# Kernel optimization log

Hardware: AMD Instinct MI355X
Metric: run time of the kernel (lower is better)

The kernel has to match this reference:

```python
import jax, jax.numpy as jnp
import numpy as np

B, P = 4, 2048
N = B * P
QD = 512            # query_dim == inner_dim (pos_emb is added to raw features)
CD = 512            # context_dim
HEADS, DH = 8, 64
INNER = HEADS * DH
SCALE = DH ** -0.5
HC, WC = 32, 32     # context spatial grid
L = HC * WC         # context_len
SELF_HW = 512       # spatial_dim[:2]
STRIDE = 8          # resolution_level == sparse tensor stride
PE_H = SELF_HW // STRIDE  # 64 BEV pos-emb grid


def setup_inputs() -> dict:
    key = jax.random.key(0)
    k = jax.random.split(key, 9)
    return {
        "feats": jax.random.normal(k[0], (N, QD), jnp.float32),
        "coords_xy": jax.random.randint(k[1], (N, 2), 0, SELF_HW),
        "context_emb": jax.random.normal(k[2], (B, HC, WC, CD), jnp.float32),
        "Wq": jax.random.normal(k[3], (QD, INNER), jnp.float32) * 0.02,
        "Wk": jax.random.normal(k[4], (CD, INNER), jnp.float32) * 0.02,
        "Wv": jax.random.normal(k[5], (CD, INNER), jnp.float32) * 0.02,
        "Wo": jax.random.normal(k[6], (INNER, QD), jnp.float32) * 0.02,
        "bo": jnp.zeros((QD,), jnp.float32),
        "pos_embedding": jax.random.normal(k[7], (PE_H, PE_H, INNER), jnp.float32) / INNER ** 0.5,
        "context_pos_embedding": jax.random.normal(k[8], (L, CD), jnp.float32) / INNER ** 0.5,
    }


def _neighbor_mask(coords_xy):
    # get_context_mask: scatter a (2*STRIDE+1)^2 neighborhood around each point's
    # projected context cell into a [N, L] boolean mask
    ratio = jnp.float32(HC) / jnp.float32(SELF_HW)
    center = jnp.round(coords_xy.astype(jnp.float32) * ratio).astype(jnp.int32)  # [N,2]
    off = jnp.stack(
        jnp.meshgrid(jnp.arange(-STRIDE, STRIDE + 1), jnp.arange(-STRIDE, STRIDE + 1), indexing="ij"),
        axis=-1,
    ).reshape(-1, 2)  # [K,2], K = 289
    pos = center[:, None, :] + off[None, :, :]        # [N,K,2]
    r = jnp.clip(pos[..., 0], 0, HC - 1)
    c = jnp.clip(pos[..., 1], 0, WC - 1)
    flat = r * WC + c                                  # [N,K]
    return jnp.zeros((N, L), jnp.bool_).at[jnp.arange(N)[:, None], flat].set(True)


def reference(feats, coords_xy, context_emb, Wq, Wk, Wv, Wo, bo, pos_embedding, context_pos_embedding):
    # get_context: add learned context positional embedding, flatten spatial -> [B, L, CD]
    ctx = (context_emb + context_pos_embedding.reshape(HC, WC, CD)).reshape(B, L, CD)
    # get_pos_emb: gather BEV positional embedding per point via floor(coord/stride)
    rc = coords_xy // STRIDE                           # [N,2] in [0, 64)
    pe = pos_embedding[rc[:, 0], rc[:, 1]]             # [N, INNER]
    f = (feats + pe).reshape(B, P, QD)                 # points grouped per batch (equal counts)
    mask = _neighbor_mask(coords_xy).reshape(B, P, L)
    q = (f @ Wq).reshape(B, P, HEADS, DH).transpose(0, 2, 1, 3)    # [B,h,P,d]
    k = (ctx @ Wk).reshape(B, L, HEADS, DH).transpose(0, 2, 1, 3)  # [B,h,L,d]
    v = (ctx @ Wv).reshape(B, L, HEADS, DH).transpose(0, 2, 1, 3)
    sim = jnp.einsum("bhid,bhjd->bhij", q, k) * SCALE              # [B,h,P,L]
    neg = -jnp.finfo(sim.dtype).max
    sim = jnp.where(mask[:, None, :, :], sim, neg)
    attn = jax.nn.softmax(sim, axis=-1)
    out = jnp.einsum("bhij,bhjd->bhid", attn, v)
    out = out.transpose(0, 2, 1, 3).reshape(B, P, INNER)
    out = out @ Wo + bo                                # to_out (dropout=0, eval)
    return out.reshape(N, QD)                          # scatter back to point features
```

## Files before the change

kernel.cpp:

```cpp
#include <hip/hip_runtime.h>


typedef __attribute__((ext_vector_type(8))) short bf16x8;
typedef __attribute__((ext_vector_type(4))) float f32x4;

#define SCL 0.18033688f

__device__ __forceinline__ unsigned short f2bf(float x) {
  union { float f; unsigned int u; } v; v.f = x;
  unsigned int r = v.u + 0x7FFFu + ((v.u >> 16) & 1u);
  return (unsigned short)(r >> 16);
}

__device__ __forceinline__ unsigned int pk2bf(float a, float b) {
  return (unsigned)f2bf(a) | ((unsigned)f2bf(b) << 16);
}

__device__ __forceinline__ unsigned int cvtpk(float a, float b) {
  unsigned int r;
  asm("v_cvt_pk_bf16_f32 %0, %1, %2" : "=v"(r) : "v"(a), "v"(b));
  return r;
}

__device__ __forceinline__ float fexp2(float x) {
#if __has_builtin(__builtin_amdgcn_exp2f)
  return __builtin_amdgcn_exp2f(x);
#else
  return exp2f(x);
#endif
}

__device__ __forceinline__ void gload16(const unsigned short* g, char* l) {
  __builtin_amdgcn_global_load_lds(
      (const __attribute__((address_space(1))) unsigned int*)g,
      (__attribute__((address_space(3))) unsigned int*)l, 16, 0, 0);
}

__device__ __forceinline__ int swzb(int row, int chk) {
  return row * 128 + ((chk * 16) ^ ((row & 7) << 4));
}

__global__ __launch_bounds__(256) void prep_w(const float* __restrict__ Wq, const float* __restrict__ Wk,
                                              const float* __restrict__ Wv, const float* __restrict__ Wo,
                                              unsigned short* __restrict__ Wqt, unsigned short* __restrict__ Wkt,
                                              unsigned short* __restrict__ Wvt, unsigned short* __restrict__ Wot) {
  __shared__ float tile[64][65];
  const int bid = blockIdx.x;
  const int wsel = bid >> 6, tt = bid & 63;
  const int kt = (tt >> 3) << 6, ntb = (tt & 7) << 6;
  const float* W = (wsel == 0) ? Wq : (wsel == 1) ? Wk : (wsel == 2) ? Wv : Wo;
  unsigned short* Wt = (wsel == 0) ? Wqt : (wsel == 1) ? Wkt : (wsel == 2) ? Wvt : Wot;
  const int t = threadIdx.x;
#pragma unroll
  for (int p = 0; p < 16; ++p) {
    int e = p * 256 + t;
    int row = e >> 6, col = e & 63;
    tile[row][col] = W[(long)(kt + row) * 512 + ntb + col];
  }
  __syncthreads();
#pragma unroll
  for (int p = 0; p < 16; ++p) {
    int e = p * 256 + t;
    int n = e >> 6, k = e & 63;
    Wt[(long)(ntb + n) * 512 + kt + k] = f2bf(tile[k][n]);
  }
}

__global__ __launch_bounds__(256) void prep_in(const float* __restrict__ feats,
                                               const int* __restrict__ coords,
                                               const float* __restrict__ pos_emb,
                                               const float* __restrict__ ctx,
                                               const float* __restrict__ ctx_pos,
                                               unsigned short* __restrict__ Aq,
                                               unsigned short* __restrict__ Ac,
                                               int* __restrict__ perm) {
  if (blockIdx.x >= 6144) {
    __shared__ int hist[64];
    __shared__ int base[64];
    const int bb = blockIdx.x - 6144;
    const int t = threadIdx.x;
    if (t < 64) hist[t] = 0;
    __syncthreads();
    int keys[8];
#pragma unroll
    for (int i = 0; i < 8; ++i) {
      int q = bb * 2048 + t * 8 + i;
      int cr = (int)rintf((float)coords[2 * q] * 0.0625f);
      keys[i] = cr;
      atomicAdd(&hist[cr], 1);
    }
    __syncthreads();
    if (t == 0) {
      int s = 0;
      for (int k2 = 0; k2 < 64; ++k2) { base[k2] = s; s += hist[k2]; }
    }
    __syncthreads();
#pragma unroll
    for (int i = 0; i < 8; ++i) {
      int pos = atomicAdd(&base[keys[i]], 1);
      perm[bb * 2048 + pos] = t * 8 + i;
    }
    return;
  }
  int i = blockIdx.x * 256 + threadIdx.x;
  if (i < 1048576) {
    int e = i << 2;
    int q = e >> 9, k = e & 511;
    int pi = ((coords[2 * q] >> 3) << 6) + (coords[2 * q + 1] >> 3);
    float4 a = *(const float4*)(feats + e);
    float4 p = *(const float4*)(pos_emb + ((size_t)pi << 9) + k);
    uint2 o;
    o.x = pk2bf(a.x + p.x, a.y + p.y);
    o.y = pk2bf(a.z + p.z, a.w + p.w);
    *(uint2*)(Aq + e) = o;
  } else {
    int e = (i - 1048576) << 2;
    int r = e >> 9, k = e & 511;
    float4 a = *(const float4*)(ctx + e);
    float4 p = *(const float4*)(ctx_pos + ((size_t)(r & 1023) << 9) + k);
    uint2 o;
    o.x = pk2bf(a.x + p.x, a.y + p.y);
    o.y = pk2bf(a.z + p.z, a.w + p.w);
    *(uint2*)(Ac + e) = o;
  }
}

__global__ __launch_bounds__(256) void gemm_qkv(const unsigned short* __restrict__ Aq,
                                                const unsigned short* __restrict__ Ac,
                                                const unsigned short* __restrict__ Wqt,
                                                const unsigned short* __restrict__ Wkt,
                                                const unsigned short* __restrict__ Wvt,
                                                unsigned short* __restrict__ Qb,
                                                unsigned short* __restrict__ Kb,
                                                unsigned short* __restrict__ Vt) {
  __shared__ char Asf[2][16384];
  __shared__ char Bsf[2][16384];
  const int t = threadIdx.x, l = t & 63, wv = t >> 6;
  const int wr = (wv >> 1) << 6, wc = (wv & 1) << 6;
  const int orig = blockIdx.x;
  const int bx = (orig & 7) * 64 + (orig >> 3);
  const bool isQ = bx < 256;
  long tm; const unsigned short* Bt; const unsigned short* Ab; bool isV = false; int nt;
  if (isQ) {
    tm = (long)(bx >> 2) * 128;
    nt = bx & 3;
    Bt = Wqt + (long)nt * 65536;
    Ab = Aq;
  } else {
    const int kvx = bx - 256;
    tm = (long)(kvx >> 3) * 128;
    const int y = kvx & 7;
    isV = y >= 4; nt = y & 3;
    Bt = (isV ? Wvt : Wkt) + (long)nt * 65536;
    Ab = Ac;
  }

  const int rr = l >> 3, chs = (l & 7) ^ rr;
  auto STAGE = [&](int buf, int k0) {
#pragma unroll
    for (int i = 0; i < 4; ++i) {
      int c = (wv << 2) + i;
      int row = (c << 3) + rr;
      gload16(Ab + (tm + row) * 512 + k0 + chs * 8, Asf[buf] + (c << 10));
      gload16(Bt + (long)row * 512 + k0 + chs * 8, Bsf[buf] + (c << 10));
    }
  };

  STAGE(0, 0);
  __syncthreads();

  f32x4 acc[4][4] = {};
  const int lr = l & 15, g = l >> 4;

  for (int s = 0; s < 8; ++s) {
    const int cur = s & 1;
    if (s < 7) STAGE(cur ^ 1, (s + 1) << 6);
#pragma unroll
    for (int kk = 0; kk < 2; ++kk) {
      const int chd = (kk << 2) + g;
      bf16x8 af[4], bfr[4];
#pragma unroll
      for (int i = 0; i < 4; ++i) {
        int ra = wr + i * 16 + lr;
        int rb = wc + i * 16 + lr;
        af[i]  = *(const bf16x8*)(Asf[cur] + swzb(ra, chd));
        bfr[i] = *(const bf16x8*)(Bsf[cur] + swzb(rb, chd));
      }
#pragma unroll
      for (int mi = 0; mi < 4; ++mi)
#pragma unroll
        for (int ni = 0; ni < 4; ++ni)
          acc[mi][ni] = __builtin_amdgcn_mfma_f32_16x16x32_bf16(af[mi], bfr[ni], acc[mi][ni], 0, 0, 0);
    }
    __syncthreads();
  }

  const int lq = g << 2;
#pragma unroll
  for (int mi = 0; mi < 4; ++mi)
#pragma unroll
    for (int ni = 0; ni < 4; ++ni) {
      int cn = nt * 128 + wc + ni * 16 + lr;
      long r0 = tm + wr + mi * 16 + lq;
      if (isQ) {
#pragma unroll
        for (int r = 0; r < 4; ++r)
          Qb[(r0 + r) * 512 + cn] = f2bf(acc[mi][ni][r] * SCL);
      } else if (!isV) {
#pragma unroll
        for (int r = 0; r < 4; ++r)
          Kb[(r0 + r) * 512 + cn] = f2bf(acc[mi][ni][r]);
      } else {
        int h = cn >> 6, d = cn & 63;
#pragma unroll
        for (int r = 0; r < 4; ++r) {
          long row = r0 + r;
          int b = (int)(row >> 10), j = (int)(row & 1023);
          int jp = (j & ~63) | ((j & 15) << 2) | ((j >> 4) & 3);
          Vt[((long)(b * 8 + h) * 64 + d) * 1024 + jp] = f2bf(acc[mi][ni][r]);
        }
      }
    }
}

__global__ __launch_bounds__(512, 4) void attn_mfma(const unsigned short* __restrict__ Qb,
                                                    const unsigned short* __restrict__ Kb,
                                                    const unsigned short* __restrict__ Vt,
                                                    const int* __restrict__ coords,
                                                    const int* __restrict__ perm,
                                                    unsigned short* __restrict__ Abf) {
  __shared__ char Kl[2][8192];
  __shared__ char Vl[2][8192];
  __shared__ char Ol[2048];
  __shared__ unsigned short Plds[8][16][72];
  __shared__ int permL[128];
  __shared__ int rng[2];
  const int t = threadIdx.x, w = t >> 6, l = t & 63;
  const int g = l >> 4, lc = l & 15;
  const int orig = blockIdx.x;
  const int sw = (orig & 7) * 64 + (orig >> 3);
  const int qx = sw & 15, bh = sw >> 4;
  const int b = bh >> 3, h = bh & 7;

  if (t < 128) permL[t] = perm[b * 2048 + qx * 128 + t];
  if (t == 0) { rng[0] = 63; rng[1] = 0; }
  __syncthreads();

  int rm[4], cm[4];
  int lrmin = 63, lrmax = 0;
#pragma unroll
  for (int r = 0; r < 4; ++r) {
    long qq = (long)b * 2048 + permL[w * 16 + g * 4 + r];
    int cr = (int)rintf((float)coords[2 * qq] * 0.0625f);
    int cc = (int)rintf((float)coords[2 * qq + 1] * 0.0625f);
    int rlo = max(0, cr - 8), rhi = min(31, cr + 8);
    int clo = max(0, cc - 8), chi = min(31, cc + 8);
    rm[r] = (int)((((unsigned)1 << (rhi - rlo + 1)) - 1) << rlo);
    cm[r] = (int)((((unsigned)1 << (chi - clo + 1)) - 1) << clo);
    lrmin = min(lrmin, rlo); lrmax = max(lrmax, rhi);
  }
#pragma unroll
  for (int off = 32; off > 0; off >>= 1) {
    lrmin = min(lrmin, __shfl_xor(lrmin, off));
    lrmax = max(lrmax, __shfl_xor(lrmax, off));
  }
  const int wt0 = lrmin >> 1, wt1 = lrmax >> 1;
  if (l == 0) { atomicMin(&rng[0], lrmin); atomicMax(&rng[1], lrmax); }

  bf16x8 qfr[2];
  {
    long qrow = (long)b * 2048 + permL[w * 16 + lc];
#pragma unroll
    for (int dc = 0; dc < 2; ++dc)
      qfr[dc] = *(const bf16x8*)(Qb + qrow * 512 + h * 64 + dc * 32 + g * 8);
  }

  const int srow = t >> 3, schk = t & 7;
  const unsigned short* Kg = Kb + ((long)b * 1024) * 512 + h * 64;
  const unsigned short* Vg = Vt + ((long)bh * 64) * 1024;

  if (t < 128) {
    int r = t >> 3, c = t & 7;
    unsigned short vv = (r == 0) ? (unsigned short)0x3F80 : (unsigned short)0;
    unsigned short tmp[8] = {vv, vv, vv, vv, vv, vv, vv, vv};
    *(int4*)(Ol + swzb(r, c)) = *(int4*)tmp;
  }
  __syncthreads();
  const int t0 = rng[0] >> 1, t1 = rng[1] >> 1;
  {
    const int kb0 = t0 * 64;
    int4 sk = *(const int4*)(Kg + (long)(kb0 + srow) * 512 + schk * 8);
    int4 sv_ = *(const int4*)(Vg + (long)srow * 1024 + kb0 + schk * 8);
    *(int4*)(Kl[0] + swzb(srow, schk)) = sk;
    *(int4*)(Vl[0] + swzb(srow, schk)) = sv_;
  }
  __syncthreads();

  f32x4 po[5] = {};

  for (int kt = t0; kt <= t1; ++kt) {
    const int cur = (kt - t0) & 1;
    const int kb = kt * 64;
    int4 nk = {}, nv = {};
    if (kt < t1) {
      const int kbn = kb + 64;
      nk = *(const int4*)(Kg + (long)(kbn + srow) * 512 + schk * 8);
      nv = *(const int4*)(Vg + (long)srow * 1024 + kbn + schk * 8);
    }

    if (kt >= wt0 && kt <= wt1) {
      bf16x8 kfr[4][2];
#pragma unroll
      for (int kf = 0; kf < 4; ++kf)
#pragma unroll
        for (int dc = 0; dc < 2; ++dc)
          kfr[kf][dc] = *(const bf16x8*)(Kl[cur] + swzb(kf * 16 + lc, dc * 4 + g));

      f32x4 sv[4];
#pragma unroll
      for (int kf = 0; kf < 4; ++kf) {
        f32x4 a = {};
        a = __builtin_amdgcn_mfma_f32_16x16x32_bf16(qfr[0], kfr[kf][0], a, 0, 0, 0);
        a = __builtin_amdgcn_mfma_f32_16x16x32_bf16(qfr[1], kfr[kf][1], a, 0, 0, 0);
        sv[kf] = a;
      }

      const int jrb = kb >> 5;
      int cmk[4][4];
#pragma unroll
      for (int kf = 0; kf < 4; ++kf) {
        int jr = jrb + (kf >> 1);
#pragma unroll
        for (int r = 0; r < 4; ++r)
          cmk[kf][r] = ((rm[r] >> jr) & 1) ? cm[r] : 0;
      }
#pragma unroll
      for (int kf = 0; kf < 4; ++kf) {
        int jc = ((kf & 1) << 4) + lc;
#pragma unroll
        for (int r = 0; r < 4; ++r) {
          float p = fexp2(sv[kf][r]);
          sv[kf][r] = ((cmk[kf][r] >> jc) & 1) ? p : 0.0f;
        }
      }

      bf16x8 vfr[5][2];
#pragma unroll
      for (int df = 0; df < 4; ++df)
#pragma unroll
        for (int kc = 0; kc < 2; ++kc)
          vfr[df][kc] = *(const bf16x8*)(Vl[cur] + swzb(df * 16 + lc, kc * 4 + g));
#pragma unroll
      for (int kc = 0; kc < 2; ++kc)
        vfr[4][kc] = *(const bf16x8*)(Ol + swzb(lc, kc * 4 + g));

#pragma unroll
      for (int r = 0; r < 4; ++r) {
        uint2 pk;
        pk.x = cvtpk(sv[0][r], sv[1][r]);
        pk.y = cvtpk(sv[2][r], sv[3][r]);
        *(uint2*)(&Plds[w][g * 4 + r][4 * lc]) = pk;
      }

      bf16x8 pa0 = *(const bf16x8*)(&Plds[w][lc][g * 8]);
      bf16x8 pa1 = *(const bf16x8*)(&Plds[w][lc][32 + g * 8]);
      __builtin_amdgcn_s_setprio(1);
#pragma unroll
      for (int df = 0; df < 5; ++df) {
        po[df] = __builtin_amdgcn_mfma_f32_16x16x32_bf16(pa0, vfr[df][0], po[df], 0, 0, 0);
        po[df] = __builtin_amdgcn_mfma_f32_16x16x32_bf16(pa1, vfr[df][1], po[df], 0, 0, 0);
      }
      __builtin_amdgcn_s_setprio(0);
    }

    if (kt < t1) {
      const int nxt = cur ^ 1;
      *(int4*)(Kl[nxt] + swzb(srow, schk)) = nk;
      *(int4*)(Vl[nxt] + swzb(srow, schk)) = nv;
    }
    __syncthreads();
  }

#pragma unroll
  for (int r = 0; r < 4; ++r) {
    float lsum = __shfl(po[4][r], l & 48);
    float inv = 1.0f / lsum;
    long qr = (long)b * 2048 + permL[w * 16 + g * 4 + r];
#pragma unroll
    for (int df = 0; df < 4; ++df)
      Abf[qr * 512 + h * 64 + df * 16 + lc] = f2bf(po[df][r] * inv);
  }
}

__global__ __launch_bounds__(256) void gemm_o(const unsigned short* __restrict__ A,
                                              const unsigned short* __restrict__ Bt,
                                              float* __restrict__ C,
                                              const float* __restrict__ bias) {
  __shared__ char Asf[2][8192];
  __shared__ char Bsf[2][16384];
  const int t = threadIdx.x, l = t & 63, wv = t >> 6;
  const int wr = (wv >> 1) << 5;
  const int wc = (wv & 1) << 6;
  const int orig = blockIdx.x;
  const int bx = (orig & 7) * 64 + (orig >> 3);
  const long tm = (long)(bx >> 2) * 64;
  const long tn = (long)(bx & 3) * 128;

  const int rr = l >> 3, chs = (l & 7) ^ rr;
  auto STAGE = [&](int buf, int k0) {
#pragma unroll
    for (int i = 0; i < 2; ++i) {
      int c = (wv << 1) + i;
      int row = (c << 3) + rr;
      gload16(A + (tm + row) * 512 + k0 + chs * 8, Asf[buf] + (c << 10));
    }
#pragma unroll
    for (int i = 0; i < 4; ++i) {
      int c = (wv << 2) + i;
      int row = (c << 3) + rr;
      gload16(Bt + (tn + row) * 512 + k0 + chs * 8, Bsf[buf] + (c << 10));
    }
  };

  STAGE(0, 0);
  __syncthreads();

  f32x4 acc[2][4] = {};
  const int lr = l & 15, g = l >> 4;

  for (int s = 0; s < 8; ++s) {
    const int cur = s & 1;
    if (s < 7) STAGE(cur ^ 1, (s + 1) << 6);
#pragma unroll
    for (int kk = 0; kk < 2; ++kk) {
      const int chd = (kk << 2) + g;
      bf16x8 af[2], bfr[4];
#pragma unroll
      for (int i = 0; i < 2; ++i)
        af[i] = *(const bf16x8*)(Asf[cur] + swzb(wr + i * 16 + lr, chd));
#pragma unroll
      for (int i = 0; i < 4; ++i)
        bfr[i] = *(const bf16x8*)(Bsf[cur] + swzb(wc + i * 16 + lr, chd));
#pragma unroll
      for (int mi = 0; mi < 2; ++mi)
#pragma unroll
        for (int ni = 0; ni < 4; ++ni)
          acc[mi][ni] = __builtin_amdgcn_mfma_f32_16x16x32_bf16(af[mi], bfr[ni], acc[mi][ni], 0, 0, 0);
    }
    __syncthreads();
  }

  const int lq = g << 2;
#pragma unroll
  for (int mi = 0; mi < 2; ++mi)
#pragma unroll
    for (int ni = 0; ni < 4; ++ni) {
      long col = tn + wc + ni * 16 + lr;
      float bv = bias[col];
      long r0 = tm + wr + mi * 16 + lq;
#pragma unroll
      for (int r = 0; r < 4; ++r)
        C[(r0 + r) * 512 + col] = acc[mi][ni][r] + bv;
    }
}

extern "C" void kernel_launch(void* const* d_in, const int* in_sizes, int n_in,
                              void* d_out, int out_size, void* d_ws, size_t ws_size,
                              hipStream_t stream) {
  (void)in_sizes; (void)n_in; (void)out_size; (void)ws_size;
  const float* feats   = (const float*)d_in[0];
  const int*   coords  = (const int*)d_in[1];
  const float* ctx     = (const float*)d_in[2];
  const float* Wq      = (const float*)d_in[3];
  const float* Wk      = (const float*)d_in[4];
  const float* Wv      = (const float*)d_in[5];
  const float* Wo      = (const float*)d_in[6];
  const float* bo      = (const float*)d_in[7];
  const float* pos_emb = (const float*)d_in[8];
  const float* ctx_pos = (const float*)d_in[9];
  float* out = (float*)d_out;
  char* ws = (char*)d_ws;

  unsigned short* Wqt = (unsigned short*)(ws);
  unsigned short* Wkt = (unsigned short*)(ws + 524288);
  unsigned short* Wvt = (unsigned short*)(ws + 1048576);
  unsigned short* Wot = (unsigned short*)(ws + 1572864);
  unsigned short* Aq  = (unsigned short*)(ws + 2097152);
  unsigned short* Ac  = (unsigned short*)(ws + 10485760);
  unsigned short* Qb  = (unsigned short*)(ws + 14680064);
  unsigned short* Kb  = (unsigned short*)(ws + 23068672);
  unsigned short* Vt  = (unsigned short*)(ws + 27262976);
  unsigned short* Abf = (unsigned short*)(ws + 31457280);
  int*            prm = (int*)(ws + 39845888);

  prep_w  <<<256, 256, 0, stream>>>(Wq, Wk, Wv, Wo, Wqt, Wkt, Wvt, Wot);
  prep_in <<<6148, 256, 0, stream>>>(feats, coords, pos_emb, ctx, ctx_pos, Aq, Ac, prm);
  gemm_qkv<<<512, 256, 0, stream>>>(Aq, Ac, Wqt, Wkt, Wvt, Qb, Kb, Vt);
  attn_mfma<<<512, 512, 0, stream>>>(Qb, Kb, Vt, coords, prm, Abf);
  gemm_o  <<<512, 256, 0, stream>>>(Abf, Wot, out, bo);
}
```

Baseline: 80.69 us.

## Merge prep kernels, halve GEMM K-tile to 32, and raise MFMA priority in attention

Fuses the weight-transpose and input-prep kernels into a single launch to save one kernel launch and its tail. Both GEMMs now stage K tiles of 32 instead of 64 through LDS, with a new 4-row swizzle. This halves shared memory use, which may allow more blocks per CU, but doubles the number of loop iterations and barriers. The attention QK MFMA section is wrapped in s_setprio to favour matrix issue.

```diff
diff --git a/kernel.cpp b/kernel.cpp
--- a/kernel.cpp
+++ b/kernel.cpp
@@ -39,46 +39,49 @@
 __device__ __forceinline__ int swzb(int row, int chk) {
   return row * 128 + ((chk * 16) ^ ((row & 7) << 4));
 }
-
-__global__ __launch_bounds__(256) void prep_w(const float* __restrict__ Wq, const float* __restrict__ Wk,
-                                              const float* __restrict__ Wv, const float* __restrict__ Wo,
-                                              unsigned short* __restrict__ Wqt, unsigned short* __restrict__ Wkt,
-                                              unsigned short* __restrict__ Wvt, unsigned short* __restrict__ Wot) {
-  __shared__ float tile[64][65];
+__device__ __forceinline__ int swz32(int row, int chk) {
+  return row * 64 + ((chk << 4) ^ ((row & 3) << 4));
+}
+
+__global__ __launch_bounds__(256) void prep_all(const float* __restrict__ Wq, const float* __restrict__ Wk,
+                                                const float* __restrict__ Wv, const float* __restrict__ Wo,
+                                                const float* __restrict__ feats,
+                                                const int* __restrict__ coords,
+                                                const float* __restrict__ pos_emb,
+                                                const float* __restrict__ ctx,
+                                                const float* __restrict__ ctx_pos,
+                                                unsigned short* __restrict__ Wqt, unsigned short* __restrict__ Wkt,
+                                                unsigned short* __restrict__ Wvt, unsigned short* __restrict__ Wot,
+                                                unsigned short* __restrict__ Aq,
+                                                unsigned short* __restrict__ Ac,
+                                                int* __restrict__ perm) {
   const int bid = blockIdx.x;
-  const int wsel = bid >> 6, tt = bid & 63;
-  const int kt = (tt >> 3) << 6, ntb = (tt & 7) << 6;
-  const float* W = (wsel == 0) ? Wq : (wsel == 1) ? Wk : (wsel == 2) ? Wv : Wo;
-  unsigned short* Wt = (wsel == 0) ? Wqt : (wsel == 1) ? Wkt : (wsel == 2) ? Wvt : Wot;
   const int t = threadIdx.x;
-#pragma unroll
-  for (int p = 0; p < 16; ++p) {
-    int e = p * 256 + t;
-    int row = e >> 6, col = e & 63;
-    tile[row][col] = W[(long)(kt + row) * 512 + ntb + col];
-  }
-  __syncthreads();
-#pragma unroll
-  for (int p = 0; p < 16; ++p) {
-    int e = p * 256 + t;
-    int n = e >> 6, k = e & 63;
-    Wt[(long)(ntb + n) * 512 + kt + k] = f2bf(tile[k][n]);
-  }
-}
-
-__global__ __launch_bounds__(256) void prep_in(const float* __restrict__ feats,
-                                               const int* __restrict__ coords,
-                                               const float* __restrict__ pos_emb,
-                                               const float* __restrict__ ctx,
-                                               const float* __restrict__ ctx_pos,
-                                               unsigned short* __restrict__ Aq,
-                                               unsigned short* __restrict__ Ac,
-                                               int* __restrict__ perm) {
-  if (blockIdx.x >= 6144) {
+  if (bid < 256) {
+    __shared__ float tile[64][65];
+    const int wsel = bid >> 6, tt = bid & 63;
+    const int kt = (tt >> 3) << 6, ntb = (tt & 7) << 6;
+    const float* W = (wsel == 0) ? Wq : (wsel == 1) ? Wk : (wsel == 2) ? Wv : Wo;
+    unsigned short* Wt = (wsel == 0) ? Wqt : (wsel == 1) ? Wkt : (wsel == 2) ? Wvt : Wot;
+#pragma unroll
+    for (int p = 0; p < 16; ++p) {
+      int e = p * 256 + t;
+      int row = e >> 6, col = e & 63;
+      tile[row][col] = W[(long)(kt + row) * 512 + ntb + col];
+    }
+    __syncthreads();
+#pragma unroll
+    for (int p = 0; p < 16; ++p) {
+      int e = p * 256 + t;
+      int n = e >> 6, k = e & 63;
+      Wt[(long)(ntb + n) * 512 + kt + k] = f2bf(tile[k][n]);
+    }
+    return;
+  }
+  if (bid >= 6400) {
     __shared__ int hist[64];
     __shared__ int base[64];
-    const int bb = blockIdx.x - 6144;
-    const int t = threadIdx.x;
+    const int bb = bid - 6400;
     if (t < 64) hist[t] = 0;
     __syncthreads();
     int keys[8];
@@ -102,7 +105,7 @@
     }
     return;
   }
-  int i = blockIdx.x * 256 + threadIdx.x;
+  int i = (bid - 256) * 256 + t;
   if (i < 1048576) {
     int e = i << 2;
     int q = e >> 9, k = e & 511;
@@ -133,8 +136,8 @@
                                                 unsigned short* __restrict__ Qb,
                                                 unsigned short* __restrict__ Kb,
                                                 unsigned short* __restrict__ Vt) {
-  __shared__ char Asf[2][16384];
-  __shared__ char Bsf[2][16384];
+  __shared__ char Asf[2][8192];
+  __shared__ char Bsf[2][8192];
   const int t = threadIdx.x, l = t & 63, wv = t >> 6;
   const int wr = (wv >> 1) << 6, wc = (wv & 1) << 6;
   const int orig = blockIdx.x;
@@ -155,14 +158,15 @@
     Ab = Ac;
   }
 
-  const int rr = l >> 3, chs = (l & 7) ^ rr;
   auto STAGE = [&](int buf, int k0) {
 #pragma unroll
-    for (int i = 0; i < 4; ++i) {
-      int c = (wv << 2) + i;
-      int row = (c << 3) + rr;
-      gload16(Ab + (tm + row) * 512 + k0 + chs * 8, Asf[buf] + (c << 10));
-      gload16(Bt + (long)row * 512 + k0 + chs * 8, Bsf[buf] + (c << 10));
+    for (int i = 0; i < 2; ++i) {
+      int row = i * 64 + wv * 16 + (l >> 2);
+      int chs = (l & 3) ^ (row & 3);
+      char* dst = &(Asf[buf][i * 4096 + wv * 1024]);
+      gload16(Ab + (tm + row) * 512 + k0 + chs * 8, dst);
+      char* dstB = &(Bsf[buf][i * 4096 + wv * 1024]);
+      gload16(Bt + (long)row * 512 + k0 + chs * 8, dstB);
     }
   };
 
@@ -172,26 +176,20 @@
   f32x4 acc[4][4] = {};
   const int lr = l & 15, g = l >> 4;
 
-  for (int s = 0; s < 8; ++s) {
+  for (int s = 0; s < 16; ++s) {
     const int cur = s & 1;
-    if (s < 7) STAGE(cur ^ 1, (s + 1) << 6);
-#pragma unroll
-    for (int kk = 0; kk < 2; ++kk) {
-      const int chd = (kk << 2) + g;
-      bf16x8 af[4], bfr[4];
-#pragma unroll
-      for (int i = 0; i < 4; ++i) {
-        int ra = wr + i * 16 + lr;
-        int rb = wc + i * 16 + lr;
-        af[i]  = *(const bf16x8*)(Asf[cur] + swzb(ra, chd));
-        bfr[i] = *(const bf16x8*)(Bsf[cur] + swzb(rb, chd));
-      }
-#pragma unroll
-      for (int mi = 0; mi < 4; ++mi)
-#pragma unroll
-        for (int ni = 0; ni < 4; ++ni)
-          acc[mi][ni] = __builtin_amdgcn_mfma_f32_16x16x32_bf16(af[mi], bfr[ni], acc[mi][ni], 0, 0, 0);
-    }
+    if (s < 15) STAGE(cur ^ 1, (s + 1) << 5);
+    bf16x8 af[4], bfr[4];
+#pragma unroll
+    for (int i = 0; i < 4; ++i) {
+      af[i]  = *(const bf16x8*)(Asf[cur] + swz32(wr + i * 16 + lr, g));
+      bfr[i] = *(const bf16x8*)(Bsf[cur] + swz32(wc + i * 16 + lr, g));
+    }
+#pragma unroll
+    for (int mi = 0; mi < 4; ++mi)
+#pragma unroll
+      for (int ni = 0; ni < 4; ++ni)
+        acc[mi][ni] = __builtin_amdgcn_mfma_f32_16x16x32_bf16(af[mi], bfr[ni], acc[mi][ni], 0, 0, 0);
     __syncthreads();
   }
 
@@ -317,6 +315,7 @@
           kfr[kf][dc] = *(const bf16x8*)(Kl[cur] + swzb(kf * 16 + lc, dc * 4 + g));
 
       f32x4 sv[4];
+      __builtin_amdgcn_s_setprio(1);
 #pragma unroll
       for (int kf = 0; kf < 4; ++kf) {
         f32x4 a = {};
@@ -324,6 +323,7 @@
         a = __builtin_amdgcn_mfma_f32_16x16x32_bf16(qfr[1], kfr[kf][1], a, 0, 0, 0);
         sv[kf] = a;
       }
+      __builtin_amdgcn_s_setprio(0);
 
       const int jrb = kb >> 5;
       int cmk[4][4];
@@ -396,8 +396,8 @@
                                               const unsigned short* __restrict__ Bt,
                                               float* __restrict__ C,
                                               const float* __restrict__ bias) {
-  __shared__ char Asf[2][8192];
-  __shared__ char Bsf[2][16384];
+  __shared__ char Asf[2][4096];
+  __shared__ char Bsf[2][8192];
   const int t = threadIdx.x, l = t & 63, wv = t >> 6;
   const int wr = (wv >> 1) << 5;
   const int wc = (wv & 1) << 6;
@@ -406,19 +406,19 @@
   const long tm = (long)(bx >> 2) * 64;
   const long tn = (long)(bx & 3) * 128;
 
-  const int rr = l >> 3, chs = (l & 7) ^ rr;
   auto STAGE = [&](int buf, int k0) {
+    {
+      int row = wv * 16 + (l >> 2);
+      int chs = (l & 3) ^ (row & 3);
+      char* dst = &(Asf[buf][wv * 1024]);
+      gload16(A + (tm + row) * 512 + k0 + chs * 8, dst);
+    }
 #pragma unroll
     for (int i = 0; i < 2; ++i) {
-      int c = (wv << 1) + i;
-      int row = (c << 3) + rr;
-      gload16(A + (tm + row) * 512 + k0 + chs * 8, Asf[buf] + (c << 10));
-    }
-#pragma unroll
-    for (int i = 0; i < 4; ++i) {
-      int c = (wv << 2) + i;
-      int row = (c << 3) + rr;
-      gload16(Bt + (tn + row) * 512 + k0 + chs * 8, Bsf[buf] + (c << 10));
+      int row = i * 64 + wv * 16 + (l >> 2);
+      int chs = (l & 3) ^ (row & 3);
+      char* dst = &(Bsf[buf][i * 4096 + wv * 1024]);
+      gload16(Bt + (tn + row) * 512 + k0 + chs * 8, dst);
     }
   };
 
@@ -428,25 +428,21 @@
   f32x4 acc[2][4] = {};
   const int lr = l & 15, g = l >> 4;
 
-  for (int s = 0; s < 8; ++s) {
+  for (int s = 0; s < 16; ++s) {
     const int cur = s & 1;
-    if (s < 7) STAGE(cur ^ 1, (s + 1) << 6);
-#pragma unroll
-    for (int kk = 0; kk < 2; ++kk) {
-      const int chd = (kk << 2) + g;
-      bf16x8 af[2], bfr[4];
-#pragma unroll
-      for (int i = 0; i < 2; ++i)
-        af[i] = *(const bf16x8*)(Asf[cur] + swzb(wr + i * 16 + lr, chd));
-#pragma unroll
-      for (int i = 0; i < 4; ++i)
-        bfr[i] = *(const bf16x8*)(Bsf[cur] + swzb(wc + i * 16 + lr, chd));
-#pragma unroll
-      for (int mi = 0; mi < 2; ++mi)
-#pragma unroll
-        for (int ni = 0; ni < 4; ++ni)
-          acc[mi][ni] = __builtin_amdgcn_mfma_f32_16x16x32_bf16(af[mi], bfr[ni], acc[mi][ni], 0, 0, 0);
-    }
+    if (s < 15) STAGE(cur ^ 1, (s + 1) << 5);
+    bf16x8 af[2], bfr[4];
+#pragma unroll
+    for (int i = 0; i < 2; ++i)
+      af[i] = *(const bf16x8*)(Asf[cur] + swz32(wr + i * 16 + lr, g));
+#pragma unroll
+    for (int i = 0; i < 4; ++i)
+      bfr[i] = *(const bf16x8*)(Bsf[cur] + swz32(wc + i * 16 + lr, g));
+#pragma unroll
+    for (int mi = 0; mi < 2; ++mi)
+#pragma unroll
+      for (int ni = 0; ni < 4; ++ni)
+        acc[mi][ni] = __builtin_amdgcn_mfma_f32_16x16x32_bf16(af[mi], bfr[ni], acc[mi][ni], 0, 0, 0);
     __syncthreads();
   }
 
@@ -493,8 +489,8 @@
   unsigned short* Abf = (unsigned short*)(ws + 31457280);
   int*            prm = (int*)(ws + 39845888);
 
-  prep_w  <<<256, 256, 0, stream>>>(Wq, Wk, Wv, Wo, Wqt, Wkt, Wvt, Wot);
-  prep_in <<<6148, 256, 0, stream>>>(feats, coords, pos_emb, ctx, ctx_pos, Aq, Ac, prm);
+  prep_all<<<6404, 256, 0, stream>>>(Wq, Wk, Wv, Wo, feats, coords, pos_emb, ctx, ctx_pos,
+                                     Wqt, Wkt, Wvt, Wot, Aq, Ac, prm);
   gemm_qkv<<<512, 256, 0, stream>>>(Aq, Ac, Wqt, Wkt, Wvt, Qb, Kb, Vt);
   attn_mfma<<<512, 512, 0, stream>>>(Qb, Kb, Vt, coords, prm, Abf);
   gemm_o  <<<512, 256, 0, stream>>>(Abf, Wot, out, bo);
```

Result: no change. 80.38 us (-0.4%).
